# Kernel tuning notes

Measured on AMD Instinct MI355X. Metric: run time of the kernel, lower is better.

The kernel has to match this reference:

```python
import jax, jax.numpy as jnp
import numpy as np

B, N, D, NUM_CLASSES = 2048, 32768, 256, 100

def setup_inputs() -> dict:
    key = jax.random.key(0)
    k1, k2, k3 = jax.random.split(key, 3)
    x = jax.random.normal(k1, (B, D), dtype=jnp.float32)
    support_embeddings = jax.random.normal(k2, (N, D), dtype=jnp.float32)
    support_labels = jax.random.randint(k3, (N,), 0, NUM_CLASSES, dtype=jnp.int64)
    return {
        "x": x,
        "support_embeddings": support_embeddings,
        "support_labels": support_labels,
        "num_classes": NUM_CLASSES,
    }

def reference(x, support_embeddings, support_labels, num_classes):
    # Pairwise L2 distance [B, N] via ||q||^2 + ||s||^2 - 2 q.s (avoids [B,N,D] broadcast)
    q2 = jnp.sum(x * x, axis=1, keepdims=True)                 # [B, 1]
    s2 = jnp.sum(support_embeddings * support_embeddings, axis=1)  # [N]
    cross = jnp.einsum('bd,nd->bn', x, support_embeddings)     # [B, N]
    dist = jnp.sqrt(jnp.maximum(q2 + s2[None, :] - 2.0 * cross, 0.0))
    # topk(-dist, k=1) over support axis -> nearest neighbor index
    _, idx = jax.lax.top_k(-dist, 1)                           # [B, 1]
    idx = jnp.squeeze(idx, axis=1)                             # [B]
    labels = jnp.take(support_labels, idx, axis=0)             # [B]
    one_hot = jax.nn.one_hot(labels, num_classes, dtype=jnp.int32)  # [B, num_classes]
    return one_hot
```

## Files before the change

### kernel.cpp

```cpp
#include <hip/hip_runtime.h>

#define BQ 2048
#define NS 32768
#define DIM 256
#define NROWS (NS + BQ)

#define BMQ 256
#define BNS 128
#define BK 32
#define NST (DIM / BK)
#define GY (NS / BNS)
#define GX (BQ / BMQ)
#define EPS 0.08f

typedef _Float16 f16;
typedef _Float16 f16x4 __attribute__((ext_vector_type(4)));
typedef _Float16 f16x8 __attribute__((ext_vector_type(8)));
typedef float    f32x4 __attribute__((ext_vector_type(4)));

__device__ __forceinline__ void gload16(const f16* g, f16* l) {
    __builtin_amdgcn_global_load_lds(
        (const __attribute__((address_space(1))) unsigned int*)g,
        (__attribute__((address_space(3))) unsigned int*)l, 16, 0, 0);
}

__device__ __forceinline__ const f16x8* fragp(const f16* base, int row, int q) {
    return (const f16x8*)(base + row * 32 + ((q ^ ((row >> 1) & 3)) << 3));
}

__global__ __launch_bounds__(256) void convert_kernel(
    const float* __restrict__ x, const float* __restrict__ sup,
    f16* __restrict__ xh, f16* __restrict__ sh, float* __restrict__ s2) {
    const int wave = threadIdx.x >> 6, lane = threadIdx.x & 63;
    const int row = blockIdx.x * 4 + wave;
    if (row < NS) {
        float4 v = ((const float4*)(sup + (size_t)row * DIM))[lane];
        f16x4 hi;
        hi[0] = (f16)v.x; hi[1] = (f16)v.y; hi[2] = (f16)v.z; hi[3] = (f16)v.w;
        *(f16x4*)(sh + (size_t)row * DIM + lane * 4) = hi;
        float sum = v.x * v.x + v.y * v.y + v.z * v.z + v.w * v.w;
#pragma unroll
        for (int off = 32; off > 0; off >>= 1) sum += __shfl_xor(sum, off);
        if (lane == 0) s2[row] = sum;
    } else {
        const int q = row - NS;
        float4 v = ((const float4*)(x + (size_t)q * DIM))[lane];
        f16x4 hi;
        hi[0] = (f16)v.x; hi[1] = (f16)v.y; hi[2] = (f16)v.z; hi[3] = (f16)v.w;
        *(f16x4*)(xh + (size_t)q * DIM + lane * 4) = hi;
    }
}

__global__ __launch_bounds__(256, 2) void knn_mfma(
    const f16* __restrict__ xh, const f16* __restrict__ sh,
    const float* __restrict__ s2g,
    float* __restrict__ pv1, float* __restrict__ pv2, int* __restrict__ pi1) {
    __shared__ f16 T[3][(BMQ + BNS) * 32];

    const int tid  = threadIdx.x;
    const int lane = tid & 63, wid = tid >> 6;
    const int l16  = lane & 15, quad = lane >> 4;

    const int id   = blockIdx.y * GX + blockIdx.x;
    const int xcd  = id & 7;
    const int slot = id >> 3;
    const int gx   = slot & (GX - 1);
    const int gy   = xcd * (GY / 8) + (slot >> 3);
    const int m0   = gx * BMQ;
    const int n0   = gy * BNS;

    const int rl = lane >> 2;
    const int qs = (lane & 3) ^ ((rl >> 1) & 3);
    const size_t srcoff = (size_t)rl * DIM + qs * 8;

    const f16* px0 = xh + (size_t)(m0 + wid * 64) * DIM + srcoff;
    const f16* px1 = px0 + (size_t)16 * DIM;
    const f16* px2 = px0 + (size_t)32 * DIM;
    const f16* px3 = px0 + (size_t)48 * DIM;
    const f16* ps0 = sh + (size_t)(n0 + wid * 32) * DIM + srcoff;
    const f16* ps1 = ps0 + (size_t)16 * DIM;
    const int dX = wid * 2048;
    const int dS = BMQ * 32 + wid * 1024;

    f32x4 acc[4][8];
#pragma unroll
    for (int fi = 0; fi < 4; ++fi)
#pragma unroll
        for (int fj = 0; fj < 8; ++fj) acc[fi][fj] = (f32x4){0.f, 0.f, 0.f, 0.f};

    auto issue = [&](int s) {
        f16* base = &T[s % 3][0];
        f16* bx = base + dX;
        f16* bs = base + dS;
        const int k0 = s * BK;
        gload16(px0 + k0, bx);
        gload16(px1 + k0, bx + 512);
        gload16(px2 + k0, bx + 1024);
        gload16(px3 + k0, bx + 1536);
        gload16(ps0 + k0, bs);
        gload16(ps1 + k0, bs + 512);
    };

    issue(0);
    issue(1);

#pragma unroll
    for (int s = 0; s < NST; ++s) {
        if (s < NST - 1)
            asm volatile("s_waitcnt vmcnt(6)\n\ts_barrier" ::: "memory");
        else
            asm volatile("s_waitcnt vmcnt(0)\n\ts_barrier" ::: "memory");
        if (s + 2 < NST) issue(s + 2);

        const f16* TX = &T[s % 3][0];
        const f16* TS = TX + BMQ * 32;
        f16x8 A0 = *fragp(TX, wid * 64 + l16,      quad);
        f16x8 A1 = *fragp(TX, wid * 64 + 16 + l16, quad);
        f16x8 A2 = *fragp(TX, wid * 64 + 32 + l16, quad);
        f16x8 A3 = *fragp(TX, wid * 64 + 48 + l16, quad);
#pragma unroll
        for (int fj = 0; fj < 8; ++fj) {
            f16x8 B = *fragp(TS, fj * 16 + l16, quad);
            acc[0][fj] = __builtin_amdgcn_mfma_f32_16x16x32_f16(A0, B, acc[0][fj], 0, 0, 0);
            acc[1][fj] = __builtin_amdgcn_mfma_f32_16x16x32_f16(A1, B, acc[1][fj], 0, 0, 0);
            acc[2][fj] = __builtin_amdgcn_mfma_f32_16x16x32_f16(A2, B, acc[2][fj], 0, 0, 0);
            acc[3][fj] = __builtin_amdgcn_mfma_f32_16x16x32_f16(A3, B, acc[3][fj], 0, 0, 0);
        }
    }

    float s2v[8];
#pragma unroll
    for (int fj = 0; fj < 8; ++fj) s2v[fj] = s2g[n0 + fj * 16 + l16];
#pragma unroll
    for (int fi = 0; fi < 4; ++fi)
#pragma unroll
        for (int rg = 0; rg < 4; ++rg) {
            float bv1 = 3.4e38f, bv2 = 3.4e38f; int bi = 0;
#pragma unroll
            for (int fj = 0; fj < 8; ++fj) {
                float s = fmaf(-2.f, acc[fi][fj][rg], s2v[fj]);
                bv2 = fminf(bv2, fmaxf(bv1, s));
                bi  = (s < bv1) ? (n0 + fj * 16 + l16) : bi;
                bv1 = fminf(bv1, s);
            }
#pragma unroll
            for (int m = 1; m < 16; m <<= 1) {
                float ov1 = __shfl_xor(bv1, m);
                float ov2 = __shfl_xor(bv2, m);
                int   oi  = __shfl_xor(bi, m);
                float nb2 = fminf(fminf(bv2, ov2), fmaxf(bv1, ov1));
                bi  = (ov1 < bv1) ? oi : bi;
                bv1 = fminf(bv1, ov1);
                bv2 = nb2;
            }
            if (l16 == 0) {
                const int row = m0 + wid * 64 + fi * 16 + quad * 4 + rg;
                pv1[(size_t)row * GY + gy] = bv1;
                pv2[(size_t)row * GY + gy] = bv2;
                pi1[(size_t)row * GY + gy] = bi;
            }
        }
}

__global__ __launch_bounds__(128) void finalize_fused(
    const float* __restrict__ pv1, const float* __restrict__ pv2,
    const int* __restrict__ pi1, const float* __restrict__ x,
    const float* __restrict__ sup, const float* __restrict__ s2,
    const int* __restrict__ labels, const int* __restrict__ ncp,
    int* __restrict__ out) {
    const int q = blockIdx.x, tid = threadIdx.x;
    const int lane = tid & 63, w = tid >> 6;
    __shared__ float s_b1, s_b2;
    __shared__ int   s_bi;
    __shared__ float wv[2];
    __shared__ int   wi[2];
    __shared__ int   s_lbl;

    if (w == 0) {
        float bv1 = 3.4e38f, bv2 = 3.4e38f; int bi = 0;
        for (int t = lane; t < GY; t += 64) {
            float ov1 = pv1[(size_t)q * GY + t];
            float ov2 = pv2[(size_t)q * GY + t];
            int   oi  = pi1[(size_t)q * GY + t];
            float nb2 = fminf(fminf(bv2, ov2), fmaxf(bv1, ov1));
            bi  = (ov1 < bv1) ? oi : bi;
            bv1 = fminf(bv1, ov1);
            bv2 = nb2;
        }
#pragma unroll
        for (int m = 1; m < 64; m <<= 1) {
            float ov1 = __shfl_xor(bv1, m);
            float ov2 = __shfl_xor(bv2, m);
            int   oi  = __shfl_xor(bi, m);
            float nb2 = fminf(fminf(bv2, ov2), fmaxf(bv1, ov1));
            bi  = (ov1 < bv1) ? oi : bi;
            bv1 = fminf(bv1, ov1);
            bv2 = nb2;
        }
        if (lane == 0) { s_b1 = bv1; s_b2 = bv2; s_bi = bi; }
    }
    __syncthreads();
    int bi = s_bi;

    if (s_b2 - s_b1 <= EPS) {
        const float qb = s_b1;
        const float4 xv = ((const float4*)(x + (size_t)q * DIM))[lane];
        float best = 3.4e38f; int bn = 0x7fffffff;
        for (int c = 0; c < GY; ++c) {
            if (pv1[(size_t)q * GY + c] > qb + EPS) continue;
            const int base = c * BNS + w * 64;
#pragma unroll 4
            for (int r = 0; r < 64; ++r) {
                const int n = base + r;
                float4 sv = ((const float4*)(sup + (size_t)n * DIM))[lane];
                float d = fmaf(sv.x, xv.x,
                          fmaf(sv.y, xv.y,
                          fmaf(sv.z, xv.z, sv.w * xv.w)));
#pragma unroll
                for (int m = 32; m > 0; m >>= 1) d += __shfl_xor(d, m);
                float sc = s2[n] - 2.f * d;
                if (sc < best) { best = sc; bn = n; }
            }
        }
        if (lane == 0) { wv[w] = best; wi[w] = bn; }
        __syncthreads();
        if (tid == 0) {
            float bv = wv[0]; int bx = wi[0];
            if (wv[1] < bv || (wv[1] == bv && wi[1] < bx)) { bx = wi[1]; }
            s_bi = bx;
        }
        __syncthreads();
        bi = s_bi;
    }

    if (tid == 0) {
        bool is64 = true;
        for (int i = 1; i < 128; i += 2)
            if (labels[i] != 0) { is64 = false; break; }
        s_lbl = is64 ? labels[2 * bi] : labels[bi];
    }
    __syncthreads();
    const int nc = ncp[0], lbl = s_lbl;
    for (int c = tid; c < nc; c += 128)
        out[q * nc + c] = (c == lbl) ? 1 : 0;
}

#define SBM 128
#define SBN 128
#define SBK 16
#define SNT 4
#define SGY (NS / (SBN * SNT))
#define SLDT (SBM + 4)

__global__ __launch_bounds__(256) void s2_kernel(const float* __restrict__ s,
                                                 float* __restrict__ s2) {
    int wave = threadIdx.x >> 6, lane = threadIdx.x & 63;
    int row = blockIdx.x * 4 + wave;
    const float4* p = (const float4*)(s + (size_t)row * DIM);
    float4 v = p[lane];
    float sum = v.x * v.x + v.y * v.y + v.z * v.z + v.w * v.w;
#pragma unroll
    for (int off = 32; off > 0; off >>= 1) sum += __shfl_xor(sum, off);
    if (lane == 0) s2[row] = sum;
}

__global__ __launch_bounds__(256) void knn_f32(const float* __restrict__ x,
                                               const float* __restrict__ sup,
                                               const float* __restrict__ s2g,
                                               float* __restrict__ pvals,
                                               int* __restrict__ pidx) {
    __shared__ float Xs[SBK][SLDT];
    __shared__ float Bs[SBK][SLDT];
    const int tid = threadIdx.x;
    const int tx = tid & 15, ty = tid >> 4;
    const int m0 = blockIdx.x * SBM, by = blockIdx.y;
    const int srow = tid >> 2, skq = (tid & 3) * 4;
    float rmin[8]; int ridx[8];
#pragma unroll
    for (int i = 0; i < 8; ++i) { rmin[i] = 3.4e38f; ridx[i] = 0x7fffffff; }
    const float* xr0 = x + (size_t)(m0 + srow) * DIM + skq;
    const float* xr1 = x + (size_t)(m0 + 64 + srow) * DIM + skq;
    for (int nt = 0; nt < SNT; ++nt) {
        const int n0 = (by * SNT + nt) * SBN;
        const float* sr0 = sup + (size_t)(n0 + srow) * DIM + skq;
        const float* sr1 = sup + (size_t)(n0 + 64 + srow) * DIM + skq;
        float acc[8][8];
#pragma unroll
        for (int i = 0; i < 8; ++i)
#pragma unroll
            for (int j = 0; j < 8; ++j) acc[i][j] = 0.0f;
        for (int kt = 0; kt < DIM / SBK; ++kt) {
            const int k0 = kt * SBK;
            float4 xv0 = *(const float4*)(xr0 + k0);
            float4 xv1 = *(const float4*)(xr1 + k0);
            float4 sv0 = *(const float4*)(sr0 + k0);
            float4 sv1 = *(const float4*)(sr1 + k0);
            __syncthreads();
            Xs[skq + 0][srow] = xv0.x; Xs[skq + 1][srow] = xv0.y;
            Xs[skq + 2][srow] = xv0.z; Xs[skq + 3][srow] = xv0.w;
            Xs[skq + 0][64 + srow] = xv1.x; Xs[skq + 1][64 + srow] = xv1.y;
            Xs[skq + 2][64 + srow] = xv1.z; Xs[skq + 3][64 + srow] = xv1.w;
            Bs[skq + 0][srow] = sv0.x; Bs[skq + 1][srow] = sv0.y;
            Bs[skq + 2][srow] = sv0.z; Bs[skq + 3][srow] = sv0.w;
            Bs[skq + 0][64 + srow] = sv1.x; Bs[skq + 1][64 + srow] = sv1.y;
            Bs[skq + 2][64 + srow] = sv1.z; Bs[skq + 3][64 + srow] = sv1.w;
            __syncthreads();
#pragma unroll
            for (int k = 0; k < SBK; ++k) {
                float4 a0 = *(const float4*)&Xs[k][ty * 4];
                float4 a1 = *(const float4*)&Xs[k][64 + ty * 4];
                float4 b0 = *(const float4*)&Bs[k][tx * 4];
                float4 b1 = *(const float4*)&Bs[k][64 + tx * 4];
                float a[8] = {a0.x, a0.y, a0.z, a0.w, a1.x, a1.y, a1.z, a1.w};
                float b[8] = {b0.x, b0.y, b0.z, b0.w, b1.x, b1.y, b1.z, b1.w};
#pragma unroll
                for (int i = 0; i < 8; ++i)
#pragma unroll
                    for (int j = 0; j < 8; ++j)
                        acc[i][j] = fmaf(a[i], b[j], acc[i][j]);
            }
        }
        const int nb0 = n0 + tx * 4, nb1 = n0 + 64 + tx * 4;
        float4 s20 = *(const float4*)(s2g + nb0);
        float4 s21 = *(const float4*)(s2g + nb1);
        float s2a[8] = {s20.x, s20.y, s20.z, s20.w, s21.x, s21.y, s21.z, s21.w};
        int nca[8] = {nb0, nb0 + 1, nb0 + 2, nb0 + 3, nb1, nb1 + 1, nb1 + 2, nb1 + 3};
#pragma unroll
        for (int i = 0; i < 8; ++i)
#pragma unroll
            for (int j = 0; j < 8; ++j) {
                float sc = fmaf(-2.0f, acc[i][j], s2a[j]);
                if (sc < rmin[i] || (sc == rmin[i] && nca[j] < ridx[i])) {
                    rmin[i] = sc; ridx[i] = nca[j];
                }
            }
    }
    __syncthreads();
    float* redv = (float*)Xs;
    int* redi = (int*)Bs;
#pragma unroll
    for (int i = 0; i < 8; ++i) {
        int mrow = (i < 4) ? (ty * 4 + i) : (64 + ty * 4 + (i - 4));
        redv[mrow * 16 + tx] = rmin[i];
        redi[mrow * 16 + tx] = ridx[i];
    }
    __syncthreads();
    if (tid < SBM) {
        float best = redv[tid * 16];
        int bi = redi[tid * 16];
#pragma unroll
        for (int t = 1; t < 16; ++t) {
            float v = redv[tid * 16 + t];
            int ix = redi[tid * 16 + t];
            if (v < best || (v == best && ix < bi)) { best = v; bi = ix; }
        }
        pvals[(size_t)(m0 + tid) * SGY + by] = best;
        pidx[(size_t)(m0 + tid) * SGY + by] = bi;
    }
}

__global__ __launch_bounds__(64) void finalize_f32(const float* __restrict__ pvals,
                                                   const int* __restrict__ pidx,
                                                   const int* __restrict__ labels,
                                                   const int* __restrict__ ncp,
                                                   int* __restrict__ out) {
    const int b = blockIdx.x, lane = threadIdx.x;
    float v = pvals[(size_t)b * SGY + lane];
    int ix = pidx[(size_t)b * SGY + lane];
#pragma unroll
    for (int off = 32; off > 0; off >>= 1) {
        float ov = __shfl_xor(v, off);
        int oi = __shfl_xor(ix, off);
        if (ov < v || (ov == v && oi < ix)) { v = ov; ix = oi; }
    }
    bool is64 = true;
    for (int i = 1; i < 128; i += 2)
        if (labels[i] != 0) { is64 = false; break; }
    const int lbl = is64 ? labels[2 * ix] : labels[ix];
    const int nc = ncp[0];
    for (int c = lane; c < nc; c += 64)
        out[b * nc + c] = (c == lbl) ? 1 : 0;
}

extern "C" void kernel_launch(void* const* d_in, const int* in_sizes, int n_in,
                              void* d_out, int out_size, void* d_ws, size_t ws_size,
                              hipStream_t stream) {
    const float* x      = (const float*)d_in[0];
    const float* sup    = (const float*)d_in[1];
    const int*   labels = (const int*)d_in[2];
    const int*   ncp    = (const int*)d_in[3];
    int* out = (int*)d_out;

    char* p = (char*)d_ws;
    float* s2      = (float*)p;           p += (size_t)NS * 4;
    float* pv1     = (float*)p;           p += (size_t)BQ * GY * 4;
    float* pv2     = (float*)p;           p += (size_t)BQ * GY * 4;
    int*   pi1     = (int*)p;             p += (size_t)BQ * GY * 4;
    f16*   xh      = (f16*)p;             p += (size_t)BQ * DIM * 2;
    f16*   sh      = (f16*)p;             p += (size_t)NS * DIM * 2;
    const size_t need = (size_t)(p - (char*)d_ws);

    if (ws_size >= need) {
        convert_kernel<<<NROWS / 4, 256, 0, stream>>>(x, sup, xh, sh, s2);
        dim3 grid(GX, GY);
        knn_mfma<<<grid, 256, 0, stream>>>(xh, sh, s2, pv1, pv2, pi1);
        finalize_fused<<<BQ, 128, 0, stream>>>(pv1, pv2, pi1, x, sup, s2,
                                               labels, ncp, out);
    } else {
        float* ss2   = (float*)d_ws;
        float* pvals = ss2 + NS;
        int*   pidx  = (int*)(pvals + (size_t)BQ * SGY);
        s2_kernel<<<NS / 4, 256, 0, stream>>>(sup, ss2);
        dim3 sgrid(BQ / SBM, SGY);
        knn_f32<<<sgrid, 256, 0, stream>>>(x, sup, ss2, pvals, pidx);
        finalize_f32<<<BQ, 64, 0, stream>>>(pvals, pidx, labels, ncp, out);
    }
}
```

Measured before the change: 181.4 us.

## Load query fragments directly from global into registers, shrink LDS for higher occupancy

The query (A) operand tiles are no longer staged through LDS. Each lane now loads its f16x8 MFMA fragment straight from global memory into registers every K step, and only the support tiles stay in the triple-buffered LDS ring. This shrinks shared memory per block to roughly a third, and the launch bound is raised to 3 blocks per CU to gain occupancy and cut LDS traffic. The trade-offs are strided, less coalesced global loads for A that lean on cache hits. Register pressure also tightens under the 3-wave-per-SIMD bound, which could force spills, and the hand-written vmcnt waits were adjusted to the new load order.

```diff
diff --git a/kernel.cpp b/kernel.cpp
--- a/kernel.cpp
+++ b/kernel.cpp
@@ -17,6 +17,8 @@
 typedef _Float16 f16x4 __attribute__((ext_vector_type(4)));
 typedef _Float16 f16x8 __attribute__((ext_vector_type(8)));
 typedef float    f32x4 __attribute__((ext_vector_type(4)));
+
+#define MEMFENCE asm volatile("" ::: "memory")
 
 __device__ __forceinline__ void gload16(const f16* g, f16* l) {
     __builtin_amdgcn_global_load_lds(
@@ -51,11 +53,11 @@
     }
 }
 
-__global__ __launch_bounds__(256, 2) void knn_mfma(
+__global__ __launch_bounds__(256, 3) void knn_mfma(
     const f16* __restrict__ xh, const f16* __restrict__ sh,
     const float* __restrict__ s2g,
     float* __restrict__ pv1, float* __restrict__ pv2, int* __restrict__ pi1) {
-    __shared__ f16 T[3][(BMQ + BNS) * 32];
+    __shared__ f16 T[3][BNS * 32];
 
     const int tid  = threadIdx.x;
     const int lane = tid & 63, wid = tid >> 6;
@@ -72,15 +74,11 @@
     const int rl = lane >> 2;
     const int qs = (lane & 3) ^ ((rl >> 1) & 3);
     const size_t srcoff = (size_t)rl * DIM + qs * 8;
-
-    const f16* px0 = xh + (size_t)(m0 + wid * 64) * DIM + srcoff;
-    const f16* px1 = px0 + (size_t)16 * DIM;
-    const f16* px2 = px0 + (size_t)32 * DIM;
-    const f16* px3 = px0 + (size_t)48 * DIM;
     const f16* ps0 = sh + (size_t)(n0 + wid * 32) * DIM + srcoff;
     const f16* ps1 = ps0 + (size_t)16 * DIM;
-    const int dX = wid * 2048;
-    const int dS = BMQ * 32 + wid * 1024;
+    const int dS = wid * 1024;
+
+    const f16* pA = xh + (size_t)(m0 + wid * 64 + l16) * DIM + quad * 8;
 
     f32x4 acc[4][8];
 #pragma unroll
@@ -88,36 +86,31 @@
 #pragma unroll
         for (int fj = 0; fj < 8; ++fj) acc[fi][fj] = (f32x4){0.f, 0.f, 0.f, 0.f};
 
-    auto issue = [&](int s) {
-        f16* base = &T[s % 3][0];
-        f16* bx = base + dX;
-        f16* bs = base + dS;
+    auto issueS = [&](int s) {
+        f16* bs = &T[s % 3][dS];
         const int k0 = s * BK;
-        gload16(px0 + k0, bx);
-        gload16(px1 + k0, bx + 512);
-        gload16(px2 + k0, bx + 1024);
-        gload16(px3 + k0, bx + 1536);
         gload16(ps0 + k0, bs);
         gload16(ps1 + k0, bs + 512);
     };
 
-    issue(0);
-    issue(1);
+    issueS(0);
+    issueS(1);
+    MEMFENCE;
 
 #pragma unroll
     for (int s = 0; s < NST; ++s) {
+        MEMFENCE;
+        f16x8 A0 = *(const f16x8*)(pA +  0 * DIM + s * BK);
+        f16x8 A1 = *(const f16x8*)(pA + 16 * DIM + s * BK);
+        f16x8 A2 = *(const f16x8*)(pA + 32 * DIM + s * BK);
+        f16x8 A3 = *(const f16x8*)(pA + 48 * DIM + s * BK);
         if (s < NST - 1)
             asm volatile("s_waitcnt vmcnt(6)\n\ts_barrier" ::: "memory");
         else
-            asm volatile("s_waitcnt vmcnt(0)\n\ts_barrier" ::: "memory");
-        if (s + 2 < NST) issue(s + 2);
-
-        const f16* TX = &T[s % 3][0];
-        const f16* TS = TX + BMQ * 32;
-        f16x8 A0 = *fragp(TX, wid * 64 + l16,      quad);
-        f16x8 A1 = *fragp(TX, wid * 64 + 16 + l16, quad);
-        f16x8 A2 = *fragp(TX, wid * 64 + 32 + l16, quad);
-        f16x8 A3 = *fragp(TX, wid * 64 + 48 + l16, quad);
+            asm volatile("s_waitcnt vmcnt(4)\n\ts_barrier" ::: "memory");
+        if (s + 2 < NST) issueS(s + 2);
+
+        const f16* TS = &T[s % 3][0];
 #pragma unroll
         for (int fj = 0; fj < 8; ++fj) {
             f16x8 B = *fragp(TS, fj * 16 + l16, quad);
```

After: 204.7 us. 1.13x slower.
